# Kernel optimization log

Measured on AMD Instinct MI355X. Metric: run time of the kernel, lower is better.

Reference implementation:

```python
import jax, jax.numpy as jnp
import numpy as np

H = 4  # num_heads
EPS = 1e-5


def setup_inputs() -> dict:
    key = jax.random.key(0)
    ks = jax.random.split(key, 12)
    N, C, E = 4096, 128, 131072
    x = jax.random.normal(ks[0], (N, C), dtype=jnp.float32)
    edge_index = jax.random.randint(ks[1], (2, E), 0, N, dtype=jnp.int64)
    # guarantee every row has at least one neighbor (self-loops) to avoid NaN softmax rows
    loops = jnp.arange(N, dtype=jnp.int64)
    edge_index = edge_index.at[0, :N].set(loops).at[1, :N].set(loops)
    s = 1.0 / np.sqrt(C)
    def lin(k):
        kw, kb = jax.random.split(k)
        return (jax.random.uniform(kw, (C, C), jnp.float32, -s, s),
                jax.random.uniform(kb, (C,), jnp.float32, -s, s))
    wq, bq = lin(ks[2]); wk, bk = lin(ks[3]); wv, bv = lin(ks[4]); wo, bo = lin(ks[5])
    gamma = jnp.ones((C,), jnp.float32)
    beta = jnp.zeros((C,), jnp.float32)
    return {"x": x, "edge_index": edge_index, "wq": wq, "bq": bq, "wk": wk, "bk": bk,
            "wv": wv, "bv": bv, "wo": wo, "bo": bo, "gamma": gamma, "beta": beta}


def reference(x, edge_index, wq, bq, wk, bk, wv, bv, wo, bo, gamma, beta):
    N, C = x.shape
    D = C // H
    q = (x @ wq.T + bq).reshape(N, H, D)
    k = (x @ wk.T + bk).reshape(N, H, D)
    v = (x @ wv.T + bv).reshape(N, H, D)
    scores = jnp.einsum('nhd,mhd->nhm', q, k) / jnp.sqrt(jnp.float32(D))  # [N,H,N]
    row, col = edge_index
    mask = jnp.zeros((N, N), jnp.float32).at[row, col].set(1.0)
    scores = jnp.where(mask[:, None, :] == 0, -jnp.inf, scores)
    attn = jax.nn.softmax(scores, axis=-1)  # dropout is identity in eval
    out = jnp.einsum('nhm,mhd->nhd', attn, v).reshape(N, C)
    out = out @ wo.T + bo
    y = x + out
    mu = jnp.mean(y, axis=-1, keepdims=True)
    var = jnp.var(y, axis=-1, keepdims=True)
    return (y - mu) / jnp.sqrt(var + EPS) * gamma + beta
```

## Files before the change

kernel.cpp:

```cpp
#include <hip/hip_runtime.h>

typedef unsigned long long u64;
typedef unsigned short u16;
typedef __attribute__((ext_vector_type(8))) short short8;
typedef __attribute__((ext_vector_type(4))) float f32x4;

#define C_DIM 128
#define MAXN 128

__device__ inline u16 bf16_rn(float f) {
    unsigned u = __float_as_uint(f);
    u += 0x7FFF + ((u >> 16) & 1);
    return (u16)(u >> 16);
}
__device__ inline float bf16_tof(u16 h) { return __uint_as_float(((unsigned)h) << 16); }

__global__ __launch_bounds__(256) void prep_kernel(
    const int* __restrict__ ei, int E, u64* __restrict__ bm, int wpr,
    const float* __restrict__ x, u16* __restrict__ xh, u16* __restrict__ xl, int xq,
    const float* __restrict__ wq, const float* __restrict__ wk, const float* __restrict__ wv,
    u16* __restrict__ wH, u16* __restrict__ wL,
    const float* __restrict__ wo, float* __restrict__ woT)
{
    int tid = blockIdx.x * 256 + threadIdx.x;
    if (tid < E) {
        int r = ei[tid], c = ei[E + tid];
        atomicOr(&bm[(size_t)r * wpr + (c >> 6)], 1ull << (c & 63));
    }
    if (tid < C_DIM * C_DIM) {
        int c = tid >> 7, j = tid & 127;
        woT[tid] = wo[j * C_DIM + c];
    }
    if (tid < 3 * C_DIM * C_DIM) {
        int s = tid >> 14, i = tid & 16383;
        const float* W = (s == 0) ? wq : (s == 1) ? wk : wv;
        float f = W[i];
        u16 h = bf16_rn(f);
        wH[tid] = h;
        wL[tid] = bf16_rn(f - bf16_tof(h));
    }
    if (tid < xq) {
        float4 xv = ((const float4*)x)[tid];
        ushort4 h, l;
        h.x = bf16_rn(xv.x); l.x = bf16_rn(xv.x - bf16_tof(h.x));
        h.y = bf16_rn(xv.y); l.y = bf16_rn(xv.y - bf16_tof(h.y));
        h.z = bf16_rn(xv.z); l.z = bf16_rn(xv.z - bf16_tof(h.z));
        h.w = bf16_rn(xv.w); l.w = bf16_rn(xv.w - bf16_tof(h.w));
        ((ushort4*)xh)[tid] = h;
        ((ushort4*)xl)[tid] = l;
    }
}

__global__ __launch_bounds__(256) void qkv_mfma_kernel(
    const u16* __restrict__ xh, const u16* __restrict__ xl,
    const u16* __restrict__ wH, const u16* __restrict__ wL,
    const float* __restrict__ bq, const float* __restrict__ bk, const float* __restrict__ bv,
    float* __restrict__ qo, float* __restrict__ ko, float* __restrict__ vo, int nrg)
{
    int bid = blockIdx.x;
    int s = bid / nrg;
    int rg = bid % nrg;
    int r0 = rg * 16;
    int w  = threadIdx.x >> 6;
    int l  = threadIdx.x & 63;
    int j0 = w * 32;
    int lr = l & 15;
    int kg = l >> 4;

    const u16* xhp = xh + (size_t)(r0 + lr) * C_DIM + kg * 8;
    const u16* xlp = xl + (size_t)(r0 + lr) * C_DIM + kg * 8;
    const u16* wh  = wH + (size_t)s * C_DIM * C_DIM;
    const u16* wl  = wL + (size_t)s * C_DIM * C_DIM;
    const u16* w0h = wh + (size_t)(j0 + lr) * C_DIM + kg * 8;
    const u16* w0l = wl + (size_t)(j0 + lr) * C_DIM + kg * 8;
    const u16* w1h = w0h + 16 * C_DIM;
    const u16* w1l = w0l + 16 * C_DIM;
    const float* B = (s == 0) ? bq : (s == 1) ? bk : bv;
    float*       O = (s == 0) ? qo : (s == 1) ? ko : vo;

    float b0 = B[j0 + lr], b1 = B[j0 + 16 + lr];
    f32x4 acc0 = {b0, b0, b0, b0};
    f32x4 acc1 = {b1, b1, b1, b1};

    #pragma unroll
    for (int kk = 0; kk < C_DIM; kk += 32) {
        short8 ah  = *(const short8*)(xhp + kk);
        short8 al  = *(const short8*)(xlp + kk);
        short8 bh0 = *(const short8*)(w0h + kk);
        short8 bl0 = *(const short8*)(w0l + kk);
        short8 bh1 = *(const short8*)(w1h + kk);
        short8 bl1 = *(const short8*)(w1l + kk);
        acc0 = __builtin_amdgcn_mfma_f32_16x16x32_bf16(ah, bh0, acc0, 0, 0, 0);
        acc0 = __builtin_amdgcn_mfma_f32_16x16x32_bf16(ah, bl0, acc0, 0, 0, 0);
        acc0 = __builtin_amdgcn_mfma_f32_16x16x32_bf16(al, bh0, acc0, 0, 0, 0);
        acc1 = __builtin_amdgcn_mfma_f32_16x16x32_bf16(ah, bh1, acc1, 0, 0, 0);
        acc1 = __builtin_amdgcn_mfma_f32_16x16x32_bf16(ah, bl1, acc1, 0, 0, 0);
        acc1 = __builtin_amdgcn_mfma_f32_16x16x32_bf16(al, bh1, acc1, 0, 0, 0);
    }
    size_t ob = (size_t)(r0 + kg * 4) * C_DIM;
    #pragma unroll
    for (int i = 0; i < 4; ++i) {
        O[ob + (size_t)i * C_DIM + j0 + lr]      = acc0[i];
        O[ob + (size_t)i * C_DIM + j0 + 16 + lr] = acc1[i];
    }
}

__global__ __launch_bounds__(512, 4) void attn_oln_kernel(
    const float* __restrict__ q, const float* __restrict__ k,
    const float* __restrict__ v, const u64* __restrict__ bm, int wpr,
    const float* __restrict__ x,
    const float* __restrict__ woT, const float* __restrict__ bo,
    const float* __restrict__ gamma, const float* __restrict__ beta,
    float* __restrict__ out)
{
    const int ROWS = 8;
    __shared__ float qs[ROWS][C_DIM];
    __shared__ float xs[ROWS][C_DIM];
    __shared__ int   lm[ROWS][MAXN];
    __shared__ float ls[ROWS][4][MAXN];
    int t = threadIdx.x;
    int n0 = blockIdx.x * ROWS;
    int wave = t >> 6, lane = t & 63;
    const float scale = 0.17677669529663687f;

    int n = n0 + wave;
    qs[wave][lane]      = q[(size_t)n * C_DIM + lane] * scale;
    qs[wave][64 + lane] = q[(size_t)n * C_DIM + 64 + lane] * scale;
    u64 bits = bm[(size_t)n * wpr + lane];
    int pc = __popcll(bits);
    int incl = pc;
    #pragma unroll
    for (int off = 1; off < 64; off <<= 1) {
        int tv = __shfl_up(incl, off);
        if (lane >= off) incl += tv;
    }
    int cnt = __shfl(incl, 63);
    int pos = incl - pc;
    u64 bb = bits;
    while (bb) {
        int b = __builtin_ctzll(bb);
        bb &= bb - 1;
        if (pos < MAXN) lm[wave][pos] = (lane << 6) + b;
        ++pos;
    }
    if (cnt > MAXN) cnt = MAXN;
    __syncthreads();
    {
        int nb = lane & 15, hh = lane >> 4;
        float4 qf[8];
        #pragma unroll
        for (int u = 0; u < 8; ++u)
            qf[u] = *(const float4*)&qs[wave][hh * 32 + u * 4];
        for (int j0 = 0; j0 < cnt; j0 += 16) {
            int jj = j0 + nb;
            if (jj < cnt) {
                const float* kr = k + (size_t)lm[wave][jj] * C_DIM + hh * 32;
                float s = 0.f;
                #pragma unroll
                for (int u = 0; u < 8; ++u) {
                    float4 k4 = *(const float4*)(kr + u * 4);
                    s += qf[u].x * k4.x + qf[u].y * k4.y
                       + qf[u].z * k4.z + qf[u].w * k4.w;
                }
                ls[wave][hh][jj] = s;
            }
        }
    }
    __syncthreads();
    int g = lane >> 4, li = lane & 15;
    float mx = -1e30f;
    for (int jj = li; jj < cnt; jj += 16) mx = fmaxf(mx, ls[wave][g][jj]);
    #pragma unroll
    for (int off = 8; off; off >>= 1) mx = fmaxf(mx, __shfl_xor(mx, off));
    float sum = 0.f;
    for (int jj = li; jj < cnt; jj += 16) {
        float e = __expf(ls[wave][g][jj] - mx);
        ls[wave][g][jj] = e;
        sum += e;
    }
    #pragma unroll
    for (int off = 8; off; off >>= 1) sum += __shfl_xor(sum, off);
    float sinv = 1.0f / sum;
    __syncthreads();
    int h0 = lane >> 5;
    float s0 = __shfl(sinv, h0 * 16);
    float s1 = __shfl(sinv, (h0 + 2) * 16);
    float a0 = 0.f, a1 = 0.f;
    for (int j0 = 0; j0 < cnt; j0 += 16) {
        int cc = cnt - j0; if (cc > 16) cc = 16;
        float v0a[16], v1a[16];
        #pragma unroll
        for (int u = 0; u < 16; ++u) {
            if (u < cc) {
                int m = lm[wave][j0 + u];
                v0a[u] = v[(size_t)m * C_DIM + lane];
                v1a[u] = v[(size_t)m * C_DIM + 64 + lane];
            }
        }
        #pragma unroll
        for (int u = 0; u < 16; ++u) {
            if (u < cc) {
                a0 += ls[wave][h0][j0 + u] * v0a[u];
                a1 += ls[wave][h0 + 2][j0 + u] * v1a[u];
            }
        }
    }
    xs[wave][lane]      = a0 * s0;
    xs[wave][64 + lane] = a1 * s1;
    __syncthreads();
    int r  = t >> 6;
    int j2 = (t & 63) << 1;
    float2 acc = *(const float2*)(bo + j2);
    #pragma unroll 2
    for (int c = 0; c < C_DIM; c += 4) {
        #pragma unroll
        for (int u = 0; u < 4; ++u) {
            float2 w2 = *(const float2*)(woT + (size_t)(c + u) * C_DIM + j2);
            float xv = xs[r][c + u];
            acc.x += xv * w2.x;
            acc.y += xv * w2.y;
        }
    }
    __syncthreads();
    {
        float2 xr = *(const float2*)(x + (size_t)(n0 + r) * C_DIM + j2);
        xs[r][j2]     = acc.x + xr.x;
        xs[r][j2 + 1] = acc.y + xr.y;
    }
    __syncthreads();
    {
        float y0 = xs[wave][lane], y1 = xs[wave][64 + lane];
        float s = y0 + y1, s2 = y0 * y0 + y1 * y1;
        #pragma unroll
        for (int off = 32; off; off >>= 1) {
            s  += __shfl_xor(s, off);
            s2 += __shfl_xor(s2, off);
        }
        float mu = s * (1.0f / 128.0f);
        float var = s2 * (1.0f / 128.0f) - mu * mu;
        float rstd = rsqrtf(var + 1e-5f);
        size_t o = (size_t)n * C_DIM;
        out[o + lane]      = (y0 - mu) * rstd * gamma[lane] + beta[lane];
        out[o + 64 + lane] = (y1 - mu) * rstd * gamma[64 + lane] + beta[64 + lane];
    }
}

extern "C" void kernel_launch(void* const* d_in, const int* in_sizes, int n_in,
                              void* d_out, int out_size, void* d_ws, size_t ws_size,
                              hipStream_t stream)
{
    const float* x     = (const float*)d_in[0];
    const int*   ei    = (const int*)d_in[1];
    const float* wq    = (const float*)d_in[2];
    const float* bq    = (const float*)d_in[3];
    const float* wk    = (const float*)d_in[4];
    const float* bk    = (const float*)d_in[5];
    const float* wv    = (const float*)d_in[6];
    const float* bv    = (const float*)d_in[7];
    const float* wo    = (const float*)d_in[8];
    const float* bo    = (const float*)d_in[9];
    const float* gamma = (const float*)d_in[10];
    const float* beta  = (const float*)d_in[11];
    float* out = (float*)d_out;

    int N = in_sizes[0] / C_DIM;
    int E = in_sizes[1] / 2;
    int wpr = N >> 6;

    size_t MB = 1 << 20;
    char* base = (char*)d_ws;
    float* q   = (float*)(base + 0 * MB);
    float* k   = (float*)(base + 2 * MB);
    float* v   = (float*)(base + 4 * MB);
    u64*   bm  = (u64*)(base + 6 * MB);
    float* woT = (float*)(base + 8 * MB);
    u16*   xh  = (u16*)(base + 9 * MB);
    u16*   xl  = (u16*)(base + 10 * MB);
    u16*   wH  = (u16*)(base + 11 * MB);
    u16*   wL  = (u16*)(base + 11 * MB + 512 * 1024);

    hipMemsetAsync(bm, 0, (size_t)N * wpr * sizeof(u64), stream);

    int xq = N * C_DIM / 4;
    int nwork = (E > xq) ? E : xq;
    prep_kernel<<<(nwork + 255) / 256, 256, 0, stream>>>(
        ei, E, bm, wpr, x, xh, xl, xq, wq, wk, wv, wH, wL, wo, woT);

    int nrg = N / 16;
    qkv_mfma_kernel<<<3 * nrg, 256, 0, stream>>>(
        xh, xl, wH, wL, bq, bk, bv, q, k, v, nrg);

    attn_oln_kernel<<<N / 8, 512, 0, stream>>>(q, k, v, bm, wpr,
                                               x, woT, bo, gamma, beta, out);
}
```

Before: 130.5 us.

## Split attention and output projection, use split-bf16 MFMA for Wo GEMM

Splits the fused attention plus output-projection kernel in two. Attention writes its result as split bf16 hi/lo, and a new MFMA kernel does the Wo projection, residual add and LayerNorm. This replaces the scalar fp32 Wo loop, and the query scale moves into the QKV epilogue. The attention kernel also batches K loads two neighbours at a time, prefetches V into registers as float2 per lane, and drops several block barriers, at the cost of an extra launch and a global round trip for the attention output.

```diff
diff --git a/kernel.cpp b/kernel.cpp
--- a/kernel.cpp
+++ b/kernel.cpp
@@ -18,22 +18,18 @@
 __global__ __launch_bounds__(256) void prep_kernel(
     const int* __restrict__ ei, int E, u64* __restrict__ bm, int wpr,
     const float* __restrict__ x, u16* __restrict__ xh, u16* __restrict__ xl, int xq,
-    const float* __restrict__ wq, const float* __restrict__ wk, const float* __restrict__ wv,
-    u16* __restrict__ wH, u16* __restrict__ wL,
-    const float* __restrict__ wo, float* __restrict__ woT)
+    const float* __restrict__ wq, const float* __restrict__ wk,
+    const float* __restrict__ wv, const float* __restrict__ wo,
+    u16* __restrict__ wH, u16* __restrict__ wL)
 {
     int tid = blockIdx.x * 256 + threadIdx.x;
     if (tid < E) {
         int r = ei[tid], c = ei[E + tid];
         atomicOr(&bm[(size_t)r * wpr + (c >> 6)], 1ull << (c & 63));
     }
-    if (tid < C_DIM * C_DIM) {
-        int c = tid >> 7, j = tid & 127;
-        woT[tid] = wo[j * C_DIM + c];
-    }
-    if (tid < 3 * C_DIM * C_DIM) {
+    if (tid < 4 * C_DIM * C_DIM) {
         int s = tid >> 14, i = tid & 16383;
-        const float* W = (s == 0) ? wq : (s == 1) ? wk : wv;
+        const float* W = (s == 0) ? wq : (s == 1) ? wk : (s == 2) ? wv : wo;
         float f = W[i];
         u16 h = bf16_rn(f);
         wH[tid] = h;
@@ -77,6 +73,7 @@
     const u16* w1l = w0l + 16 * C_DIM;
     const float* B = (s == 0) ? bq : (s == 1) ? bk : bv;
     float*       O = (s == 0) ? qo : (s == 1) ? ko : vo;
+    float fin = (s == 0) ? 0.17677669529663687f : 1.0f;
 
     float b0 = B[j0 + lr], b1 = B[j0 + 16 + lr];
     f32x4 acc0 = {b0, b0, b0, b0};
@@ -100,32 +97,22 @@
     size_t ob = (size_t)(r0 + kg * 4) * C_DIM;
     #pragma unroll
     for (int i = 0; i < 4; ++i) {
-        O[ob + (size_t)i * C_DIM + j0 + lr]      = acc0[i];
-        O[ob + (size_t)i * C_DIM + j0 + 16 + lr] = acc1[i];
-    }
-}
-
-__global__ __launch_bounds__(512, 4) void attn_oln_kernel(
+        O[ob + (size_t)i * C_DIM + j0 + lr]      = acc0[i] * fin;
+        O[ob + (size_t)i * C_DIM + j0 + 16 + lr] = acc1[i] * fin;
+    }
+}
+
+__global__ __launch_bounds__(512, 4) void attn_kernel(
     const float* __restrict__ q, const float* __restrict__ k,
     const float* __restrict__ v, const u64* __restrict__ bm, int wpr,
-    const float* __restrict__ x,
-    const float* __restrict__ woT, const float* __restrict__ bo,
-    const float* __restrict__ gamma, const float* __restrict__ beta,
-    float* __restrict__ out)
-{
-    const int ROWS = 8;
-    __shared__ float qs[ROWS][C_DIM];
-    __shared__ float xs[ROWS][C_DIM];
-    __shared__ int   lm[ROWS][MAXN];
-    __shared__ float ls[ROWS][4][MAXN];
+    u16* __restrict__ aoh, u16* __restrict__ aol)
+{
+    __shared__ int   lm[8][MAXN];
+    __shared__ float ls[8][4][MAXN];
     int t = threadIdx.x;
-    int n0 = blockIdx.x * ROWS;
     int wave = t >> 6, lane = t & 63;
-    const float scale = 0.17677669529663687f;
-
-    int n = n0 + wave;
-    qs[wave][lane]      = q[(size_t)n * C_DIM + lane] * scale;
-    qs[wave][64 + lane] = q[(size_t)n * C_DIM + 64 + lane] * scale;
+    int n = blockIdx.x * 8 + wave;
+
     u64 bits = bm[(size_t)n * wpr + lane];
     int pc = __popcll(bits);
     int incl = pc;
@@ -144,29 +131,43 @@
         ++pos;
     }
     if (cnt > MAXN) cnt = MAXN;
-    __syncthreads();
+
     {
         int nb = lane & 15, hh = lane >> 4;
+        const float* qp = q + (size_t)n * C_DIM + hh * 32;
         float4 qf[8];
         #pragma unroll
-        for (int u = 0; u < 8; ++u)
-            qf[u] = *(const float4*)&qs[wave][hh * 32 + u * 4];
-        for (int j0 = 0; j0 < cnt; j0 += 16) {
-            int jj = j0 + nb;
-            if (jj < cnt) {
-                const float* kr = k + (size_t)lm[wave][jj] * C_DIM + hh * 32;
-                float s = 0.f;
-                #pragma unroll
-                for (int u = 0; u < 8; ++u) {
-                    float4 k4 = *(const float4*)(kr + u * 4);
-                    s += qf[u].x * k4.x + qf[u].y * k4.y
-                       + qf[u].z * k4.z + qf[u].w * k4.w;
-                }
-                ls[wave][hh][jj] = s;
+        for (int u = 0; u < 8; ++u) qf[u] = *(const float4*)(qp + u * 4);
+        for (int j0 = 0; j0 < cnt; j0 += 32) {
+            int ja = j0 + nb, jb = j0 + 16 + nb;
+            int ma = lm[wave][ja < cnt ? ja : 0];
+            int mb = lm[wave][jb < cnt ? jb : 0];
+            const float* ka = k + (size_t)ma * C_DIM + hh * 32;
+            const float* kb = k + (size_t)mb * C_DIM + hh * 32;
+            float4 A[8], B[8];
+            #pragma unroll
+            for (int u = 0; u < 8; ++u) {
+                A[u] = *(const float4*)(ka + u * 4);
+                B[u] = *(const float4*)(kb + u * 4);
             }
-        }
-    }
-    __syncthreads();
+            float sa = 0.f, sb = 0.f;
+            #pragma unroll
+            for (int u = 0; u < 8; ++u) {
+                sa += qf[u].x * A[u].x + qf[u].y * A[u].y
+                    + qf[u].z * A[u].z + qf[u].w * A[u].w;
+                sb += qf[u].x * B[u].x + qf[u].y * B[u].y
+                    + qf[u].z * B[u].z + qf[u].w * B[u].w;
+            }
+            if (ja < cnt) ls[wave][hh][ja] = sa;
+            if (jb < cnt) ls[wave][hh][jb] = sb;
+        }
+    }
+    float2 vbuf[32];
+    #pragma unroll
+    for (int u = 0; u < 32; ++u) {
+        int m = lm[wave][u < cnt ? u : 0];
+        vbuf[u] = *(const float2*)(v + (size_t)m * C_DIM + 2 * lane);
+    }
     int g = lane >> 4, li = lane & 15;
     float mx = -1e30f;
     for (int jj = li; jj < cnt; jj += 16) mx = fmaxf(mx, ls[wave][g][jj]);
@@ -181,67 +182,109 @@
     #pragma unroll
     for (int off = 8; off; off >>= 1) sum += __shfl_xor(sum, off);
     float sinv = 1.0f / sum;
+    float2 acc = {0.f, 0.f};
+    for (int j0 = 0; j0 < cnt; j0 += 32) {
+        if (j0) {
+            #pragma unroll
+            for (int u = 0; u < 32; ++u) {
+                int jj = j0 + u;
+                int m = lm[wave][jj < cnt ? jj : 0];
+                vbuf[u] = *(const float2*)(v + (size_t)m * C_DIM + 2 * lane);
+            }
+        }
+        int cc = cnt - j0; if (cc > 32) cc = 32;
+        #pragma unroll
+        for (int u = 0; u < 32; ++u) {
+            if (u < cc) {
+                float e = ls[wave][g][j0 + u];
+                acc.x += e * vbuf[u].x;
+                acc.y += e * vbuf[u].y;
+            }
+        }
+    }
+    float f0 = acc.x * sinv, f1 = acc.y * sinv;
+    ushort2 ho, lo;
+    ho.x = bf16_rn(f0); lo.x = bf16_rn(f0 - bf16_tof(ho.x));
+    ho.y = bf16_rn(f1); lo.y = bf16_rn(f1 - bf16_tof(ho.y));
+    *(ushort2*)(aoh + (size_t)n * C_DIM + 2 * lane) = ho;
+    *(ushort2*)(aol + (size_t)n * C_DIM + 2 * lane) = lo;
+}
+
+__global__ __launch_bounds__(256) void oln_kernel(
+    const u16* __restrict__ aoh, const u16* __restrict__ aol,
+    const u16* __restrict__ woh, const u16* __restrict__ wol,
+    const float* __restrict__ bo, const float* __restrict__ x,
+    const float* __restrict__ gamma, const float* __restrict__ beta,
+    float* __restrict__ out)
+{
+    __shared__ float ys[8 * 132];
+    int r0 = blockIdx.x * 8;
+    int w  = threadIdx.x >> 6;
+    int l  = threadIdx.x & 63;
+    int j0 = w * 32;
+    int lr = l & 15;
+    int kg = l >> 4;
+    int ar = lr & 7;
+
+    const u16* ahp = aoh + (size_t)(r0 + ar) * C_DIM + kg * 8;
+    const u16* alp = aol + (size_t)(r0 + ar) * C_DIM + kg * 8;
+    const u16* w0h = woh + (size_t)(j0 + lr) * C_DIM + kg * 8;
+    const u16* w0l = wol + (size_t)(j0 + lr) * C_DIM + kg * 8;
+    const u16* w1h = w0h + 16 * C_DIM;
+    const u16* w1l = w0l + 16 * C_DIM;
+
+    float b0 = bo[j0 + lr], b1 = bo[j0 + 16 + lr];
+    f32x4 acc0 = {b0, b0, b0, b0};
+    f32x4 acc1 = {b1, b1, b1, b1};
+
+    #pragma unroll
+    for (int kk = 0; kk < C_DIM; kk += 32) {
+        short8 ah  = *(const short8*)(ahp + kk);
+        short8 al  = *(const short8*)(alp + kk);
+        short8 bh0 = *(const short8*)(w0h + kk);
+        short8 bl0 = *(const short8*)(w0l + kk);
+        short8 bh1 = *(const short8*)(w1h + kk);
+        short8 bl1 = *(const short8*)(w1l + kk);
+        acc0 = __builtin_amdgcn_mfma_f32_16x16x32_bf16(ah, bh0, acc0, 0, 0, 0);
+        acc0 = __builtin_amdgcn_mfma_f32_16x16x32_bf16(ah, bl0, acc0, 0, 0, 0);
+        acc0 = __builtin_amdgcn_mfma_f32_16x16x32_bf16(al, bh0, acc0, 0, 0, 0);
+        acc1 = __builtin_amdgcn_mfma_f32_16x16x32_bf16(ah, bh1, acc1, 0, 0, 0);
+        acc1 = __builtin_amdgcn_mfma_f32_16x16x32_bf16(ah, bl1, acc1, 0, 0, 0);
+        acc1 = __builtin_amdgcn_mfma_f32_16x16x32_bf16(al, bh1, acc1, 0, 0, 0);
+    }
+    #pragma unroll
+    for (int i = 0; i < 4; ++i) {
+        int rr = kg * 4 + i;
+        if (rr < 8) {
+            float y0 = acc0[i] + x[(size_t)(r0 + rr) * C_DIM + j0 + lr];
+            float y1 = acc1[i] + x[(size_t)(r0 + rr) * C_DIM + j0 + 16 + lr];
+            ys[rr * 132 + j0 + lr]      = y0;
+            ys[rr * 132 + j0 + 16 + lr] = y1;
+        }
+    }
     __syncthreads();
-    int h0 = lane >> 5;
-    float s0 = __shfl(sinv, h0 * 16);
-    float s1 = __shfl(sinv, (h0 + 2) * 16);
-    float a0 = 0.f, a1 = 0.f;
-    for (int j0 = 0; j0 < cnt; j0 += 16) {
-        int cc = cnt - j0; if (cc > 16) cc = 16;
-        float v0a[16], v1a[16];
-        #pragma unroll
-        for (int u = 0; u < 16; ++u) {
-            if (u < cc) {
-                int m = lm[wave][j0 + u];
-                v0a[u] = v[(size_t)m * C_DIM + lane];
-                v1a[u] = v[(size_t)m * C_DIM + 64 + lane];
-            }
-        }
-        #pragma unroll
-        for (int u = 0; u < 16; ++u) {
-            if (u < cc) {
-                a0 += ls[wave][h0][j0 + u] * v0a[u];
-                a1 += ls[wave][h0 + 2][j0 + u] * v1a[u];
-            }
-        }
-    }
-    xs[wave][lane]      = a0 * s0;
-    xs[wave][64 + lane] = a1 * s1;
-    __syncthreads();
-    int r  = t >> 6;
-    int j2 = (t & 63) << 1;
-    float2 acc = *(const float2*)(bo + j2);
-    #pragma unroll 2
-    for (int c = 0; c < C_DIM; c += 4) {
-        #pragma unroll
-        for (int u = 0; u < 4; ++u) {
-            float2 w2 = *(const float2*)(woT + (size_t)(c + u) * C_DIM + j2);
-            float xv = xs[r][c + u];
-            acc.x += xv * w2.x;
-            acc.y += xv * w2.y;
-        }
-    }
-    __syncthreads();
-    {
-        float2 xr = *(const float2*)(x + (size_t)(n0 + r) * C_DIM + j2);
-        xs[r][j2]     = acc.x + xr.x;
-        xs[r][j2 + 1] = acc.y + xr.y;
-    }
-    __syncthreads();
-    {
-        float y0 = xs[wave][lane], y1 = xs[wave][64 + lane];
-        float s = y0 + y1, s2 = y0 * y0 + y1 * y1;
-        #pragma unroll
-        for (int off = 32; off; off >>= 1) {
+    if (threadIdx.x < 128) {
+        int rr = threadIdx.x >> 4;
+        int c0 = (threadIdx.x & 15) * 8;
+        float yv[8];
+        float s = 0.f, s2 = 0.f;
+        #pragma unroll
+        for (int u = 0; u < 8; ++u) {
+            yv[u] = ys[rr * 132 + c0 + u];
+            s += yv[u]; s2 += yv[u] * yv[u];
+        }
+        #pragma unroll
+        for (int off = 8; off; off >>= 1) {
             s  += __shfl_xor(s, off);
             s2 += __shfl_xor(s2, off);
         }
         float mu = s * (1.0f / 128.0f);
         float var = s2 * (1.0f / 128.0f) - mu * mu;
         float rstd = rsqrtf(var + 1e-5f);
-        size_t o = (size_t)n * C_DIM;
-        out[o + lane]      = (y0 - mu) * rstd * gamma[lane] + beta[lane];
-        out[o + 64 + lane] = (y1 - mu) * rstd * gamma[64 + lane] + beta[64 + lane];
+        size_t o = (size_t)(r0 + rr) * C_DIM + c0;
+        #pragma unroll
+        for (int u = 0; u < 8; ++u)
+            out[o + u] = (yv[u] - mu) * rstd * gamma[c0 + u] + beta[c0 + u];
     }
 }
 
@@ -273,23 +316,27 @@
     float* k   = (float*)(base + 2 * MB);
     float* v   = (float*)(base + 4 * MB);
     u64*   bm  = (u64*)(base + 6 * MB);
-    float* woT = (float*)(base + 8 * MB);
-    u16*   xh  = (u16*)(base + 9 * MB);
-    u16*   xl  = (u16*)(base + 10 * MB);
-    u16*   wH  = (u16*)(base + 11 * MB);
-    u16*   wL  = (u16*)(base + 11 * MB + 512 * 1024);
+    u16*   xh  = (u16*)(base + 8 * MB);
+    u16*   xl  = (u16*)(base + 9 * MB);
+    u16*   wH  = (u16*)(base + 10 * MB);
+    u16*   wL  = (u16*)(base + 10 * MB + 512 * 1024);
+    u16*   aoh = (u16*)(base + 11 * MB);
+    u16*   aol = (u16*)(base + 12 * MB);
 
     hipMemsetAsync(bm, 0, (size_t)N * wpr * sizeof(u64), stream);
 
     int xq = N * C_DIM / 4;
     int nwork = (E > xq) ? E : xq;
     prep_kernel<<<(nwork + 255) / 256, 256, 0, stream>>>(
-        ei, E, bm, wpr, x, xh, xl, xq, wq, wk, wv, wH, wL, wo, woT);
+        ei, E, bm, wpr, x, xh, xl, xq, wq, wk, wv, wo, wH, wL);
 
     int nrg = N / 16;
     qkv_mfma_kernel<<<3 * nrg, 256, 0, stream>>>(
         xh, xl, wH, wL, bq, bk, bv, q, k, v, nrg);
 
-    attn_oln_kernel<<<N / 8, 512, 0, stream>>>(q, k, v, bm, wpr,
-                                               x, woT, bo, gamma, beta, out);
-}
+    attn_kernel<<<N / 8, 512, 0, stream>>>(q, k, v, bm, wpr, aoh, aol);
+
+    oln_kernel<<<N / 8, 256, 0, stream>>>(
+        aoh, aol, wH + 3 * C_DIM * C_DIM, wL + 3 * C_DIM * C_DIM,
+        bo, x, gamma, beta, out);
+}
```

Measured after the change: 126.5 us. 1.03x faster.
